# Performance work log

Measured on AMD Instinct MI355X. Metric: run time of the kernel, lower is better.

The kernel has to match this reference:

```python
import jax, jax.numpy as jnp
import numpy as np

EPS = 1e-8        # LinearGELU eps
LN_EPS = 1e-5     # LayerNorm eps
NUM_HEADS = 16
DIM = 1024
HIDDEN = 4096
B, N = 4, 785


def _lin(x, xj, w, lw, b=None, lb=None):
    # LinearLinear: primal linear + JVP wrt input and tangent params (lw, lb)
    y = x @ w.T
    yj = xj @ w.T + x @ lw.T
    if b is not None:
        y = y + b
    if lb is not None:
        yj = yj + lb
    return y, yj


def _ln(x, xj, w, b, lw, lb):
    # LinearLayerNorm forward + manual JVP (matches torch source exactly)
    mean = x.mean(-1, keepdims=True)
    xc = x - mean
    var = (xc * xc).mean(-1, keepdims=True)
    std = jnp.sqrt(var + LN_EPS)
    xhat = xc / std
    out = xhat * w + b
    t1 = xhat * lw + lb                              # tangent wrt affine params
    mj = xj.mean(-1, keepdims=True)
    xjc = xj - mj
    a = xjc * std
    corr = 2.0 * (xc * xjc).mean(-1, keepdims=True)
    bterm = (0.5 / std) * corr * xc
    c = (1.0 / std) ** 2 * (a - bterm)
    return out, t1 + c * w


def _gelu(x, xj):
    # exact (erf) GELU; jvp uses gelu(x)/(x+EPS) + x*pdf(x) as in source
    out = 0.5 * x * (1.0 + jax.lax.erf(x * np.float32(1.0 / np.sqrt(2.0))))
    pdf = jnp.exp(-0.5 * x * x) * np.float32(1.0 / np.sqrt(2.0 * np.pi))
    return out, xj * (out / (x + EPS) + x * pdf)


def _attn(x, xj, qkv_w, qkv_lw, proj_w, proj_b, proj_lw, proj_lb):
    Bb, Nn, C = x.shape
    H = NUM_HEADS
    D = C // H
    scale = np.float32(D) ** -0.5
    qkv, qkv_j = _lin(x, xj, qkv_w, qkv_lw)  # [B,N,3C], qkv_bias=False
    def split(t):
        return t.reshape(Bb, Nn, 3, H, D).transpose(2, 0, 3, 1, 4)
    q, k, v = split(qkv)
    qj, kj, vj = split(qkv_j)
    q = q * scale
    qj = qj * scale
    attn = jax.nn.softmax(jnp.einsum('bhnd,bhmd->bhnm', q, k), axis=-1)
    out = jnp.einsum('bhnm,bhmd->bhnd', attn, v)
    # softmax JVP: dm = A_jvp + B_jvp; filter = dm*attn - rowsum(dm*attn)*attn
    dm = jnp.einsum('bhnd,bhmd->bhnm', qj, k) + jnp.einsum('bhnd,bhmd->bhnm', q, kj)
    f = dm * attn
    filt = f - f.sum(-1, keepdims=True) * attn  # == diag(dm @ attn^T) * attn correction
    out_j = jnp.einsum('bhnm,bhmd->bhnd', filt, v) + jnp.einsum('bhnm,bhmd->bhnd', attn, vj)
    out = out.transpose(0, 2, 1, 3).reshape(Bb, Nn, C)
    out_j = out_j.transpose(0, 2, 1, 3).reshape(Bb, Nn, C)
    return _lin(out, out_j, proj_w, proj_lw, proj_b, proj_lb)


def setup_inputs() -> dict:
    keys = jax.random.split(jax.random.key(0), 32)
    ki = iter(keys)
    def nrm(shape, s=0.02):
        return (jax.random.normal(next(ki), shape, jnp.float32) * s).astype(jnp.float32)
    d, h = DIM, HIDDEN
    inp = {
        'input': jax.random.normal(next(ki), (B, N, d), jnp.float32),
        'input_jvp': jax.random.normal(next(ki), (B, N, d), jnp.float32),
        'n1_w': 1.0 + nrm((d,), 0.1), 'n1_b': nrm((d,), 0.1),
        'n1_lw': nrm((d,), 0.1), 'n1_lb': nrm((d,), 0.1),
        'qkv_w': nrm((3 * d, d)), 'qkv_lw': nrm((3 * d, d)),
        'proj_w': nrm((d, d)), 'proj_b': nrm((d,), 0.1),
        'proj_lw': nrm((d, d)), 'proj_lb': nrm((d,), 0.1),
        'n2_w': 1.0 + nrm((d,), 0.1), 'n2_b': nrm((d,), 0.1),
        'n2_lw': nrm((d,), 0.1), 'n2_lb': nrm((d,), 0.1),
        'fc1_w': nrm((h, d)), 'fc1_b': nrm((h,), 0.1),
        'fc1_lw': nrm((h, d)), 'fc1_lb': nrm((h,), 0.1),
        'fc2_w': nrm((d, h)), 'fc2_b': nrm((d,), 0.1),
        'fc2_lw': nrm((d, h)), 'fc2_lb': nrm((d,), 0.1),
    }
    return inp


def reference(input, input_jvp, n1_w, n1_b, n1_lw, n1_lb, qkv_w, qkv_lw,
              proj_w, proj_b, proj_lw, proj_lb, n2_w, n2_b, n2_lw, n2_lb,
              fc1_w, fc1_b, fc1_lw, fc1_lb, fc2_w, fc2_b, fc2_lw, fc2_lb):
    x, xj = _ln(input, input_jvp, n1_w, n1_b, n1_lw, n1_lb)
    x, xj = _attn(x, xj, qkv_w, qkv_lw, proj_w, proj_b, proj_lw, proj_lb)
    x = x + input
    xj = xj + input_jvp
    i2, i2j = x, xj
    x, xj = _ln(x, xj, n2_w, n2_b, n2_lw, n2_lb)
    x, xj = _lin(x, xj, fc1_w, fc1_lw, fc1_b, fc1_lb)
    x, xj = _gelu(x, xj)
    x, xj = _lin(x, xj, fc2_w, fc2_lw, fc2_b, fc2_lb)
    return (x + i2, xj + i2j)
```

## Files before the change

kernel.cpp:

```cpp
#include <hip/hip_runtime.h>
#include <hip/hip_bf16.h>

typedef unsigned short u16;
typedef unsigned int   u32;

#define MP     3328
#define MREAL  3140
#define DIMC   1024
#define H3C    3072
#define HIDC   4096
#define NKV    785
#define SLEN   896

typedef __bf16 bf16x8 __attribute__((ext_vector_type(8)));
typedef float  f32x4  __attribute__((ext_vector_type(4)));

#define MFMA(d,a,b) (d) = __builtin_amdgcn_mfma_f32_16x16x32_bf16((a),(b),(d),0,0,0)

__device__ __forceinline__ u16 f2bf(float f){
  u32 u = __builtin_bit_cast(u32, f);
  return (u16)((u + 0x7fffu + ((u >> 16) & 1u)) >> 16);
}
__device__ __forceinline__ float bf2f(u16 h){
  return __builtin_bit_cast(float, (u32)h << 16);
}
__device__ __forceinline__ void gload16(const u16* g, u16* l){
  __builtin_amdgcn_global_load_lds(
      (const __attribute__((address_space(1))) void*)g,
      (__attribute__((address_space(3))) void*)l, 16, 0, 0);
}
__device__ __forceinline__ float wsum(float v){
  #pragma unroll
  for (int o = 32; o >= 1; o >>= 1) v += __shfl_xor(v, o);
  return v;
}

__global__ __launch_bounds__(256) void cvt2_k(
    const float* __restrict__ in0, u16* __restrict__ out0, int n0,
    const float* __restrict__ in1, u16* __restrict__ out1, int n1)
{
  int i = (blockIdx.x * 256 + threadIdx.x) * 4;
  const float* src; u16* dst;
  if (i < n0){ src = in0 + i; dst = out0 + i; }
  else { int j = i - n0; if (j >= n1) return; src = in1 + j; dst = out1 + j; }
  float4 v = *(const float4*)src;
  ushort4 o4;
  o4.x = f2bf(v.x); o4.y = f2bf(v.y); o4.z = f2bf(v.z); o4.w = f2bf(v.w);
  *(ushort4*)dst = o4;
}

__global__ __launch_bounds__(256) void ln_jvp_k(
    const float* __restrict__ x, const float* __restrict__ xj,
    const float* __restrict__ w, const float* __restrict__ b,
    const float* __restrict__ lw, const float* __restrict__ lb,
    u16* __restrict__ out, u16* __restrict__ outj)
{
  const int row = blockIdx.x, t = threadIdx.x;
  const size_t ro = (size_t)row * DIMC;
  if (row >= MREAL){
    for (int i = t; i < DIMC; i += 256){ out[ro+i] = 0; outj[ro+i] = 0; }
    return;
  }
  const float4 v  = ((const float4*)(x  + ro))[t];
  const float4 vj = ((const float4*)(xj + ro))[t];
  float sx  = v.x+v.y+v.z+v.w;
  float sxx = v.x*v.x+v.y*v.y+v.z*v.z+v.w*v.w;
  float sj  = vj.x+vj.y+vj.z+vj.w;
  float sxj = v.x*vj.x+v.y*vj.y+v.z*vj.z+v.w*vj.w;
  __shared__ __attribute__((aligned(64))) float red[4][4];
  sx = wsum(sx); sxx = wsum(sxx); sj = wsum(sj); sxj = wsum(sxj);
  const int wid = t>>6, lane = t&63;
  if (lane == 0){ red[wid][0]=sx; red[wid][1]=sxx; red[wid][2]=sj; red[wid][3]=sxj; }
  __syncthreads();
  sx  = red[0][0]+red[1][0]+red[2][0]+red[3][0];
  sxx = red[0][1]+red[1][1]+red[2][1]+red[3][1];
  sj  = red[0][2]+red[1][2]+red[2][2]+red[3][2];
  sxj = red[0][3]+red[1][3]+red[2][3]+red[3][3];
  const float inv  = 1.0f/1024.0f;
  const float mean = sx*inv, meanj = sj*inv;
  const float var  = sxx*inv - mean*mean;
  const float cov  = sxj*inv - mean*meanj;
  const float rstd = rsqrtf(var + 1e-5f);
  const float r3   = rstd*rstd*rstd;
  const float4 wv  = ((const float4*)w)[t];
  const float4 bv  = ((const float4*)b)[t];
  const float4 lwv = ((const float4*)lw)[t];
  const float4 lbv = ((const float4*)lb)[t];
  const float xs[4]  = {v.x,v.y,v.z,v.w},   xjs[4] = {vj.x,vj.y,vj.z,vj.w};
  const float wss[4] = {wv.x,wv.y,wv.z,wv.w}, bs[4] = {bv.x,bv.y,bv.z,bv.w};
  const float lws[4] = {lwv.x,lwv.y,lwv.z,lwv.w}, lbs[4] = {lbv.x,lbv.y,lbv.z,lbv.w};
  const int i0 = t*4;
  #pragma unroll
  for (int e = 0; e < 4; e++){
    const float xc = xs[e]-mean, xjc = xjs[e]-meanj;
    const float xhat = xc*rstd;
    const float cc = xjc*rstd - xc*cov*r3;
    out [ro+i0+e] = f2bf(xhat*wss[e] + bs[e]);
    outj[ro+i0+e] = f2bf(xhat*lws[e] + lbs[e] + cc*wss[e]);
  }
}

template<int EPI>
__global__ __launch_bounds__(512, 1) void gemm_jvp_wide_k(
    const u16* __restrict__ A, const u16* __restrict__ Aj, int lda,
    const u16* __restrict__ B, const u16* __restrict__ Bj, int K,
    const float* __restrict__ bias, const float* __restrict__ biasj,
    void* __restrict__ Yv, void* __restrict__ Yjv, int ldy)
{
  __shared__ __attribute__((aligned(128))) u16 lds[3][24576];
  const int tid = threadIdx.x, wid = tid>>6, lane = tid&63;
  const int l4 = lane>>4, l15 = lane&15;
  const int ord = blockIdx.y * gridDim.x + blockIdx.x;
  const int cpx = (gridDim.x * gridDim.y) >> 3;
  const int nbk = (ord & 7) * cpx + (ord >> 3);
  const int m0 = (nbk / gridDim.x) * 256;
  const int n0 = (nbk % gridDim.x) * 128;
  f32x4 accY[4][4], accJ[4][4];
  #pragma unroll
  for (int i = 0; i < 4; i++)
    #pragma unroll
    for (int j = 0; j < 4; j++){
      accY[i][j] = (f32x4){0.f,0.f,0.f,0.f};
      accJ[i][j] = (f32x4){0.f,0.f,0.f,0.f};
    }
  const int boA0 = tid*16,        boA1 = (512+tid)*16;
  const int sbA0 = boA0 ^ (((boA0>>7)&7)<<4);
  const int sbA1 = boA1 ^ (((boA1>>7)&7)<<4);
  const int rA0 = sbA0>>6, cA0 = (sbA0&63)>>1;
  const int rA1 = sbA1>>6, cA1 = (sbA1&63)>>1;
  const int boB = tid*16;
  const int sbB = boB ^ (((boB>>7)&7)<<4);
  const int rB = sbB>>6, cB = (sbB&63)>>1;
  const u16* srcA0  = A  + (size_t)(m0+rA0)*lda + cA0;
  const u16* srcA1  = A  + (size_t)(m0+rA1)*lda + cA1;
  const u16* srcAj0 = Aj + (size_t)(m0+rA0)*lda + cA0;
  const u16* srcAj1 = Aj + (size_t)(m0+rA1)*lda + cA1;
  const u16* srcB   = B  + (size_t)(n0+rB)*K + cB;
  const u16* srcBj  = Bj + (size_t)(n0+rB)*K + cB;
  const int dA0 = tid*8, dA1 = (512+tid)*8, dB = tid*8;
  const int wr = wid>>1, wc = wid&1;
  int aoff[4], boff[4];
  #pragma unroll
  for (int i = 0; i < 4; i++){
    int ab_ = (wr*64 + i*16 + l15)*64 + l4*16;
    aoff[i] = ab_ ^ (((ab_>>7)&7)<<4);
    int bb_ = (wc*64 + i*16 + l15)*64 + l4*16;
    boff[i] = bb_ ^ (((bb_>>7)&7)<<4);
  }
  auto STAGE = [&](int buf, int t){
    const int k0 = t<<5;
    u16* Lb = &lds[buf][0];
    gload16(srcA0 +k0, Lb + dA0);
    gload16(srcA1 +k0, Lb + dA1);
    gload16(srcAj0+k0, Lb + 8192 + dA0);
    gload16(srcAj1+k0, Lb + 8192 + dA1);
    gload16(srcB  +k0, Lb + 16384 + dB);
    gload16(srcBj +k0, Lb + 20480 + dB);
  };
  const int nt = K >> 5;
  STAGE(0, 0);
  STAGE(1, 1);
  for (int t = 0; t < nt; t++){
    if (t + 1 < nt) asm volatile("s_waitcnt vmcnt(6)" ::: "memory");
    else            asm volatile("s_waitcnt vmcnt(0)" ::: "memory");
    __builtin_amdgcn_s_barrier();
    if (t + 2 < nt) STAGE((t+2)%3, t+2);
    const char* Lb = (const char*)&lds[t%3][0];
    bf16x8 af[4], ajf[4], bbf[4], bjf[4];
    #pragma unroll
    for (int i = 0; i < 4; i++){
      af[i]  = *(const bf16x8*)(Lb + aoff[i]);
      ajf[i] = *(const bf16x8*)(Lb + 16384 + aoff[i]);
      bbf[i] = *(const bf16x8*)(Lb + 32768 + boff[i]);
      bjf[i] = *(const bf16x8*)(Lb + 40960 + boff[i]);
    }
    __builtin_amdgcn_s_setprio(1);
    #pragma unroll
    for (int i = 0; i < 4; i++)
      #pragma unroll
      for (int j = 0; j < 4; j++){
        MFMA(accY[i][j], af[i],  bbf[j]);
        MFMA(accJ[i][j], ajf[i], bbf[j]);
        MFMA(accJ[i][j], af[i],  bjf[j]);
      }
    __builtin_amdgcn_s_setprio(0);
  }
  const int mb = m0 + wr*64 + (l4<<2);
  const int nb = n0 + wc*64 + l15;
  #pragma unroll
  for (int i = 0; i < 4; i++)
    #pragma unroll
    for (int j = 0; j < 4; j++)
      #pragma unroll
      for (int r = 0; r < 4; r++){
        const int m = mb + i*16 + r, n = nb + j*16;
        float y = accY[i][j][r], yj = accJ[i][j][r];
        if (EPI == 0){
          ((u16*)Yv )[(size_t)m*ldy+n] = f2bf(y);
          ((u16*)Yjv)[(size_t)m*ldy+n] = f2bf(yj);
        } else {
          y  += bias[n];
          yj += biasj[n];
          const float ge  = 0.5f*y*(1.0f + erff(y*0.70710678118654752f));
          const float pdf = __expf(-0.5f*y*y)*0.3989422804014327f;
          const float gj  = yj*(ge/(y + 1e-8f) + y*pdf);
          ((u16*)Yv )[(size_t)m*ldy+n] = f2bf(ge);
          ((u16*)Yjv)[(size_t)m*ldy+n] = f2bf(gj);
        }
      }
}

template<int EPI>
__global__ __launch_bounds__(256) void gemm_jvp_k(
    const u16* __restrict__ A, const u16* __restrict__ Aj, int lda,
    const u16* __restrict__ B, const u16* __restrict__ Bj, int K,
    const float* __restrict__ bias, const float* __restrict__ biasj,
    const float* __restrict__ res, const float* __restrict__ resj,
    void* __restrict__ Yv, void* __restrict__ Yjv, int ldy, int mwrite)
{
  __shared__ __attribute__((aligned(128))) u16 lds[3][4][128*32];
  const int tid = threadIdx.x, wid = tid>>6, lane = tid&63;
  const int ord = blockIdx.y * gridDim.x + blockIdx.x;
  const int cpx = (gridDim.x * gridDim.y) >> 3;
  const int nbk = (ord & 7) * cpx + (ord >> 3);
  const int m0 = (nbk / gridDim.x) * 128;
  const int n0 = (nbk % gridDim.x) * 128;
  f32x4 accY[4][4], accJ[4][4];
  #pragma unroll
  for (int i = 0; i < 4; i++)
    #pragma unroll
    for (int j = 0; j < 4; j++){
      accY[i][j] = (f32x4){0.f,0.f,0.f,0.f};
      accJ[i][j] = (f32x4){0.f,0.f,0.f,0.f};
    }
  const int bo0 = wid*1024 + lane*16;
  const int bo1 = bo0 + 4096;
  const int sb0 = bo0 ^ (((bo0>>7)&7)<<4);
  const int sb1 = bo1 ^ (((bo1>>7)&7)<<4);
  const int r0 = sb0>>6, c0 = (sb0&63)>>1;
  const int r1 = sb1>>6, c1 = (sb1&63)>>1;
  const u16* A0  = A  + (size_t)(m0+r0)*lda + c0;
  const u16* A1  = A  + (size_t)(m0+r1)*lda + c1;
  const u16* Aj0 = Aj + (size_t)(m0+r0)*lda + c0;
  const u16* Aj1 = Aj + (size_t)(m0+r1)*lda + c1;
  const u16* B0  = B  + (size_t)(n0+r0)*K + c0;
  const u16* B1  = B  + (size_t)(n0+r1)*K + c1;
  const u16* Bj0 = Bj + (size_t)(n0+r0)*K + c0;
  const u16* Bj1 = Bj + (size_t)(n0+r1)*K + c1;
  const int kq = (lane>>4)<<3;
  const int ar = (wid>>1)*64 + (lane&15);
  const int bc = (wid&1)*64 + (lane&15);
  int aoff[4], boff[4];
  #pragma unroll
  for (int i = 0; i < 4; i++){
    int ab_ = (ar+i*16)*64 + (kq<<1);
    aoff[i] = ab_ ^ (((ab_>>7)&7)<<4);
    int bb_ = (bc+i*16)*64 + (kq<<1);
    boff[i] = bb_ ^ (((bb_>>7)&7)<<4);
  }
  auto STAGE = [&](int buf, int t){
    const int k0 = t<<5;
    u16* p0 = &lds[buf][0][0];
    gload16(A0 +k0, p0+(bo0>>1)); gload16(A1 +k0, p0+(bo1>>1));
    u16* p1 = &lds[buf][1][0];
    gload16(Aj0+k0, p1+(bo0>>1)); gload16(Aj1+k0, p1+(bo1>>1));
    u16* p2 = &lds[buf][2][0];
    gload16(B0 +k0, p2+(bo0>>1)); gload16(B1 +k0, p2+(bo1>>1));
    u16* p3 = &lds[buf][3][0];
    gload16(Bj0+k0, p3+(bo0>>1)); gload16(Bj1+k0, p3+(bo1>>1));
  };
  const int nt = K >> 5;
  STAGE(0, 0);
  STAGE(1, 1);
  for (int t = 0; t < nt; t++){
    if (t + 1 < nt) asm volatile("s_waitcnt vmcnt(8)" ::: "memory");
    else            asm volatile("s_waitcnt vmcnt(0)" ::: "memory");
    __builtin_amdgcn_s_barrier();
    if (t + 2 < nt) STAGE((t+2)%3, t+2);
    const char* lAb  = (const char*)&lds[t%3][0][0];
    const char* lAjb = (const char*)&lds[t%3][1][0];
    const char* lBb  = (const char*)&lds[t%3][2][0];
    const char* lBjb = (const char*)&lds[t%3][3][0];
    bf16x8 af[4], ajf[4], bbf[4], bjf[4];
    #pragma unroll
    for (int i = 0; i < 4; i++){
      af[i]  = *(const bf16x8*)(lAb  + aoff[i]);
      ajf[i] = *(const bf16x8*)(lAjb + aoff[i]);
      bbf[i] = *(const bf16x8*)(lBb  + boff[i]);
      bjf[i] = *(const bf16x8*)(lBjb + boff[i]);
    }
    __builtin_amdgcn_s_setprio(1);
    #pragma unroll
    for (int i = 0; i < 4; i++)
      #pragma unroll
      for (int j = 0; j < 4; j++){
        MFMA(accY[i][j], af[i],  bbf[j]);
        MFMA(accJ[i][j], ajf[i], bbf[j]);
        MFMA(accJ[i][j], af[i],  bjf[j]);
      }
    __builtin_amdgcn_s_setprio(0);
  }
  const int mb = m0 + (wid>>1)*64 + ((lane>>4)<<2);
  const int nb = n0 + (wid&1)*64 + (lane&15);
  #pragma unroll
  for (int i = 0; i < 4; i++)
    #pragma unroll
    for (int j = 0; j < 4; j++)
      #pragma unroll
      for (int r = 0; r < 4; r++){
        const int m = mb + i*16 + r, n = nb + j*16;
        float y = accY[i][j][r], yj = accJ[i][j][r];
        if (EPI == 0){
          ((u16*)Yv )[(size_t)m*ldy+n] = f2bf(y);
          ((u16*)Yjv)[(size_t)m*ldy+n] = f2bf(yj);
        } else if (EPI == 1){
          if (m < mwrite){
            y  += bias[n]  + res [(size_t)m*ldy+n];
            yj += biasj[n] + resj[(size_t)m*ldy+n];
            ((float*)Yv )[(size_t)m*ldy+n] = y;
            ((float*)Yjv)[(size_t)m*ldy+n] = yj;
          }
        } else {
          y  += bias[n];
          yj += biasj[n];
          const float ge  = 0.5f*y*(1.0f + erff(y*0.70710678118654752f));
          const float pdf = __expf(-0.5f*y*y)*0.3989422804014327f;
          const float gj  = yj*(ge/(y + 1e-8f) + y*pdf);
          ((u16*)Yv )[(size_t)m*ldy+n] = f2bf(ge);
          ((u16*)Yjv)[(size_t)m*ldy+n] = f2bf(gj);
        }
      }
}

__global__ __launch_bounds__(256) void transpose_v_k(
    const u16* __restrict__ qkvb, const u16* __restrict__ qkvjb,
    u16* __restrict__ vT, u16* __restrict__ vjT)
{
  __shared__ __attribute__((aligned(64))) u16 tl[64][80];
  __shared__ __attribute__((aligned(64))) u16 tlj[64][80];
  const int kt = blockIdx.x, bh = blockIdx.y;
  const int b = bh>>4, h = bh&15;
  const int t = threadIdx.x;
  const int kv = t>>2, dd = (t&3)*16;
  const int kvg = kt*64 + kv;
  if (kvg < NKV){
    const u16* s0 = qkvb  + (size_t)(b*NKV+kvg)*H3C + 2048 + h*64 + dd;
    const u16* s1 = qkvjb + (size_t)(b*NKV+kvg)*H3C + 2048 + h*64 + dd;
    *(uint4*)&tl [kv][dd]   = *(const uint4*)s0;
    *(uint4*)&tl [kv][dd+8] = *(const uint4*)(s0+8);
    *(uint4*)&tlj[kv][dd]   = *(const uint4*)s1;
    *(uint4*)&tlj[kv][dd+8] = *(const uint4*)(s1+8);
  } else {
    uint4 z = {0,0,0,0};
    *(uint4*)&tl [kv][dd] = z; *(uint4*)&tl [kv][dd+8] = z;
    *(uint4*)&tlj[kv][dd] = z; *(uint4*)&tlj[kv][dd+8] = z;
  }
  __syncthreads();
  const int d = t>>2, kc = (t&3)*16;
  u16* d0 = vT  + ((size_t)bh*64 + d)*SLEN + kt*64 + kc;
  u16* d1 = vjT + ((size_t)bh*64 + d)*SLEN + kt*64 + kc;
  #pragma unroll
  for (int e = 0; e < 16; e++){ d0[e] = tl[kc+e][d]; d1[e] = tlj[kc+e][d]; }
}

__global__ __launch_bounds__(256) void flash_attn_jvp_k(
    const u16* __restrict__ qkvb, const u16* __restrict__ qkvjb,
    const u16* __restrict__ vT, const u16* __restrict__ vjT,
    u16* __restrict__ o, u16* __restrict__ oj)
{
  __shared__ __attribute__((aligned(128))) u16 lK  [2][64*64];
  __shared__ __attribute__((aligned(128))) u16 lKj [2][64*64];
  __shared__ __attribute__((aligned(128))) u16 lvT [64*64];
  __shared__ __attribute__((aligned(128))) u16 lvjT[64*64];
  __shared__ __attribute__((aligned(128))) u16 pl  [128*64];
  __shared__ __attribute__((aligned(128))) u16 pdl [128*64];
  const int tid = threadIdx.x, wid = tid>>6, lane = tid&63;
  const int l4 = lane>>4, l15 = lane&15;
  const int qt = blockIdx.x, bh = blockIdx.y, b = bh>>4, h = bh&15;

  bf16x8 qf[2][2], qjf[2][2];
  {
    const size_t qrb = (size_t)b*NKV + qt*128 + wid*32;
    #pragma unroll
    for (int i = 0; i < 2; i++){
      const size_t ro = (qrb + i*16 + l15)*H3C + h*64;
      #pragma unroll
      for (int ks = 0; ks < 2; ks++){
        qf [i][ks] = *(const bf16x8*)(qkvb  + ro + ks*32 + l4*8);
        qjf[i][ks] = *(const bf16x8*)(qkvjb + ro + ks*32 + l4*8);
      }
    }
  }
  float m_st[2][4], l_pt[2][4], g_pt[2][4];
  f32x4 PO[2][4], PTJ[2][4];
  #pragma unroll
  for (int i = 0; i < 2; i++)
    #pragma unroll
    for (int r = 0; r < 4; r++){
      m_st[i][r] = -1e30f; l_pt[i][r] = 0.f; g_pt[i][r] = 0.f;
    }
  #pragma unroll
  for (int i = 0; i < 2; i++)
    #pragma unroll
    for (int j = 0; j < 4; j++){
      PO[i][j] = (f32x4){0.f,0.f,0.f,0.f};
      PTJ[i][j] = (f32x4){0.f,0.f,0.f,0.f};
    }
  char* plb  = (char*)pl;
  char* pdlb = (char*)pdl;
  const char* lvTb  = (const char*)lvT;
  const char* lvjTb = (const char*)lvjT;

  const int g0 = tid, g1 = 256 + tid;
  const int row0 = g0>>3, cs0 = (g0&7) ^ (row0&7);
  const int row1 = g1>>3, cs1 = (g1&7) ^ (row1&7);
  auto stageK = [&](int buf, int t){
    const size_t k0 = (size_t)(b*NKV + t*64 + row0)*H3C + 1024 + h*64 + cs0*8;
    const size_t k1 = (size_t)(b*NKV + t*64 + row1)*H3C + 1024 + h*64 + cs1*8;
    gload16(qkvb  + k0, &lK [buf][0] + g0*8);
    gload16(qkvjb + k0, &lKj[buf][0] + g0*8);
    gload16(qkvb  + k1, &lK [buf][0] + g1*8);
    gload16(qkvjb + k1, &lKj[buf][0] + g1*8);
  };
  auto stageV = [&](int t){
    const size_t v0 = ((size_t)bh*64 + row0)*SLEN + t*64 + cs0*8;
    const size_t v1 = ((size_t)bh*64 + row1)*SLEN + t*64 + cs1*8;
    gload16(vT  + v0, lvT  + g0*8);
    gload16(vjT + v0, lvjT + g0*8);
    gload16(vT  + v1, lvT  + g1*8);
    gload16(vjT + v1, lvjT + g1*8);
  };

  stageK(0, 0);
  stageV(0);
  for (int t = 0; t < 13; t++){
    asm volatile("s_waitcnt vmcnt(4)" ::: "memory");
    __builtin_amdgcn_s_barrier();
    const char* lKb  = (const char*)&lK [t&1][0];
    const char* lKjb = (const char*)&lKj[t&1][0];

    #pragma unroll
    for (int i = 0; i < 2; i++){
      f32x4 s[4], dm[4];
      #pragma unroll
      for (int j = 0; j < 4; j++){
        s[j] = (f32x4){0.f,0.f,0.f,0.f};
        dm[j] = (f32x4){0.f,0.f,0.f,0.f};
      }
      #pragma unroll
      for (int ks = 0; ks < 2; ks++){
        #pragma unroll
        for (int j = 0; j < 4; j++){
          const int row = j*16 + l15;
          const int byt = (row*128 + ks*64 + l4*16) ^ ((row&7)<<4);
          const bf16x8 kf  = *(const bf16x8*)(lKb  + byt);
          const bf16x8 kjf = *(const bf16x8*)(lKjb + byt);
          MFMA(s[j],  qf[i][ks],  kf);
          MFMA(dm[j], qjf[i][ks], kf);
          MFMA(dm[j], qf[i][ks],  kjf);
        }
      }
      float tm[4] = {-1e30f,-1e30f,-1e30f,-1e30f};
      #pragma unroll
      for (int j = 0; j < 4; j++){
        const int colg = t*64 + j*16 + l15;
        #pragma unroll
        for (int r = 0; r < 4; r++){
          float sv = s[j][r]*0.125f;
          if (colg >= NKV) sv = -1e30f;
          s[j][r] = sv;
          dm[j][r] *= 0.125f;
          tm[r] = fmaxf(tm[r], sv);
        }
      }
      float vmax[4];
      bool need = false;
      #pragma unroll
      for (int r = 0; r < 4; r++){
        float v = tm[r];
        v = fmaxf(v, __shfl_xor(v, 1));
        v = fmaxf(v, __shfl_xor(v, 2));
        v = fmaxf(v, __shfl_xor(v, 4));
        v = fmaxf(v, __shfl_xor(v, 8));
        vmax[r] = v;
        need = need || (v > m_st[i][r] + 4.0f);
      }
      if (__any(need)){
        #pragma unroll
        for (int r = 0; r < 4; r++){
          const float nm = fmaxf(m_st[i][r], vmax[r]);
          const float sc = __expf(m_st[i][r] - nm);
          m_st[i][r] = nm;
          l_pt[i][r] *= sc;
          g_pt[i][r] *= sc;
          #pragma unroll
          for (int j = 0; j < 4; j++){ PO[i][j][r] *= sc; PTJ[i][j][r] *= sc; }
        }
      }
      #pragma unroll
      for (int j = 0; j < 4; j++){
        const int col = j*16 + l15;
        #pragma unroll
        for (int r = 0; r < 4; r++){
          const float p  = __expf(s[j][r] - m_st[i][r]);
          const float pd = p * dm[j][r];
          l_pt[i][r] += p;
          g_pt[i][r] += pd;
          const int row = wid*32 + i*16 + l4*4 + r;
          const int byt = (row*128 + col*2) ^ ((row&7)<<4);
          *(u16*)(plb  + byt) = f2bf(p);
          *(u16*)(pdlb + byt) = f2bf(pd);
        }
      }
    }

    if (t + 1 < 13) stageK((t+1)&1, t+1);
    if (t + 1 < 13) asm volatile("s_waitcnt vmcnt(4)" ::: "memory");
    else            asm volatile("s_waitcnt vmcnt(0)" ::: "memory");
    __builtin_amdgcn_s_barrier();

    #pragma unroll
    for (int ks = 0; ks < 2; ks++){
      bf16x8 pa[2], pda[2];
      #pragma unroll
      for (int i = 0; i < 2; i++){
        const int row = wid*32 + i*16 + l15;
        const int byt = (row*128 + ks*64 + l4*16) ^ ((row&7)<<4);
        pa[i]  = *(const bf16x8*)(plb  + byt);
        pda[i] = *(const bf16x8*)(pdlb + byt);
      }
      #pragma unroll
      for (int j = 0; j < 4; j++){
        const int row = j*16 + l15;
        const int byt = (row*128 + ks*64 + l4*16) ^ ((row&7)<<4);
        const bf16x8 vb  = *(const bf16x8*)(lvTb  + byt);
        const bf16x8 vjb = *(const bf16x8*)(lvjTb + byt);
        #pragma unroll
        for (int i = 0; i < 2; i++){
          MFMA(PO[i][j],  pa[i],  vb);
          MFMA(PTJ[i][j], pda[i], vb);
          MFMA(PTJ[i][j], pa[i],  vjb);
        }
      }
    }
    __builtin_amdgcn_s_barrier();
    if (t + 1 < 13) stageV(t+1);
  }

  #pragma unroll
  for (int i = 0; i < 2; i++)
    #pragma unroll
    for (int r = 0; r < 4; r++){
      float lv = l_pt[i][r], gv = g_pt[i][r];
      lv += __shfl_xor(lv, 1); gv += __shfl_xor(gv, 1);
      lv += __shfl_xor(lv, 2); gv += __shfl_xor(gv, 2);
      lv += __shfl_xor(lv, 4); gv += __shfl_xor(gv, 4);
      lv += __shfl_xor(lv, 8); gv += __shfl_xor(gv, 8);
      const int ql = qt*128 + wid*32 + i*16 + l4*4 + r;
      if (ql < NKV){
        const float rl = 1.0f / lv;
        const float gg = gv * rl;
        #pragma unroll
        for (int j = 0; j < 4; j++){
          const size_t oo = ((size_t)b*NKV + ql)*DIMC + h*64 + j*16 + l15;
          const float po = PO[i][j][r] * rl;
          o [oo] = f2bf(po);
          oj[oo] = f2bf(PTJ[i][j][r]*rl - gg*po);
        }
      }
    }
}

extern "C" void kernel_launch(void* const* d_in, const int* in_sizes, int n_in,
                              void* d_out, int out_size, void* d_ws, size_t ws_size,
                              hipStream_t stream)
{
  (void)in_sizes; (void)n_in; (void)out_size;
  const float* input   = (const float*)d_in[0];
  const float* inputj  = (const float*)d_in[1];
  const float* n1_w    = (const float*)d_in[2];
  const float* n1_b    = (const float*)d_in[3];
  const float* n1_lw   = (const float*)d_in[4];
  const float* n1_lb   = (const float*)d_in[5];
  const float* qkv_w   = (const float*)d_in[6];
  const float* qkv_lw  = (const float*)d_in[7];
  const float* proj_w  = (const float*)d_in[8];
  const float* proj_b  = (const float*)d_in[9];
  const float* proj_lw = (const float*)d_in[10];
  const float* proj_lb = (const float*)d_in[11];
  const float* n2_w    = (const float*)d_in[12];
  const float* n2_b    = (const float*)d_in[13];
  const float* n2_lw   = (const float*)d_in[14];
  const float* n2_lb   = (const float*)d_in[15];
  const float* fc1_w   = (const float*)d_in[16];
  const float* fc1_b   = (const float*)d_in[17];
  const float* fc1_lw  = (const float*)d_in[18];
  const float* fc1_lb  = (const float*)d_in[19];
  const float* fc2_w   = (const float*)d_in[20];
  const float* fc2_b   = (const float*)d_in[21];
  const float* fc2_lw  = (const float*)d_in[22];
  const float* fc2_lb  = (const float*)d_in[23];

  const size_t SZ_W      = 2u*4194304u*2u;
  const size_t SZ_ARENA1 = 2u*(size_t)MP*HIDC*2u;
  const size_t SZ_VT     = (size_t)64*64*SLEN*2u;
  const size_t SZ_ARENA2 = 2u*SZ_VT;
  const size_t SZ_ARENA3 = 2u*(size_t)MP*DIMC*2u;
  const size_t SZ_X2     = (size_t)MP*DIMC*4u;
  const size_t NEEDED = SZ_W + SZ_ARENA1 + SZ_ARENA2 + SZ_ARENA3 + 2u*SZ_X2 + 4096u;
  if (ws_size < NEEDED) return;

  char* base = (char*)d_ws;
  size_t off = 0;
  auto ab = [&](size_t bytes)->char*{
    char* p = base + off;
    off += bytes; off = (off + 255) & ~(size_t)255;
    return p;
  };
  char* Wslot  = ab(SZ_W);
  char* arena1 = ab(SZ_ARENA1);
  char* arena2 = ab(SZ_ARENA2);
  char* arena3 = ab(SZ_ARENA3);
  float* x2  = (float*)ab(SZ_X2);
  float* x2j = (float*)ab(SZ_X2);

  u16* wbuf  = (u16*)Wslot;
  u16* wjbuf = wbuf + 4194304;
  u16* qkvb  = (u16*)arena1;
  u16* qkvjb = qkvb + (size_t)MP*H3C;
  u16* hb    = (u16*)arena1;
  u16* hjb   = hb + (size_t)MP*HIDC;
  u16* vT    = (u16*)arena2;
  u16* vjT   = vT + (size_t)64*64*SLEN;
  u16* x3b   = (u16*)arena2;
  u16* x3jb  = x3b + (size_t)MP*DIMC;
  u16* x1b   = (u16*)arena3;
  u16* x1jb  = x1b + (size_t)MP*DIMC;
  u16* ob    = (u16*)arena3;
  u16* ojb   = ob + (size_t)MP*DIMC;

  auto cvt2 = [&](const float* s0, u16* d0, int n0,
                  const float* s1, u16* d1, int n1){
    cvt2_k<<<dim3((n0 + n1 + 1023)/1024), 256, 0, stream>>>(s0, d0, n0, s1, d1, n1);
  };

  ln_jvp_k<<<dim3(MP), 256, 0, stream>>>(input, inputj, n1_w, n1_b, n1_lw, n1_lb,
                                         x1b, x1jb);
  cvt2(qkv_w, wbuf, H3C*DIMC, qkv_lw, wjbuf, H3C*DIMC);
  gemm_jvp_wide_k<0><<<dim3(H3C/128, MP/256), 512, 0, stream>>>(
      x1b, x1jb, DIMC, wbuf, wjbuf, DIMC, nullptr, nullptr,
      qkvb, qkvjb, H3C);
  transpose_v_k<<<dim3(14, 64), 256, 0, stream>>>(qkvb, qkvjb, vT, vjT);
  flash_attn_jvp_k<<<dim3(7, 64), 256, 0, stream>>>(qkvb, qkvjb, vT, vjT, ob, ojb);
  cvt2(proj_w, wbuf, DIMC*DIMC, proj_lw, wjbuf, DIMC*DIMC);
  gemm_jvp_k<1><<<dim3(DIMC/128, MP/128), 256, 0, stream>>>(
      ob, ojb, DIMC, wbuf, wjbuf, DIMC, proj_b, proj_lb, input, inputj,
      x2, x2j, DIMC, MREAL);
  ln_jvp_k<<<dim3(MP), 256, 0, stream>>>(x2, x2j, n2_w, n2_b, n2_lw, n2_lb,
                                         x3b, x3jb);
  cvt2(fc1_w, wbuf, HIDC*DIMC, fc1_lw, wjbuf, HIDC*DIMC);
  gemm_jvp_wide_k<2><<<dim3(HIDC/128, MP/256), 512, 0, stream>>>(
      x3b, x3jb, DIMC, wbuf, wjbuf, DIMC, fc1_b, fc1_lb,
      hb, hjb, HIDC);
  cvt2(fc2_w, wbuf, DIMC*HIDC, fc2_lw, wjbuf, DIMC*HIDC);
  float* out0 = (float*)d_out;
  float* out1 = out0 + (size_t)MREAL*DIMC;
  gemm_jvp_k<1><<<dim3(DIMC/128, MP/128), 256, 0, stream>>>(
      hb, hjb, HIDC, wbuf, wjbuf, HIDC, fc2_b, fc2_lb, x2, x2j,
      out0, out1, DIMC, MREAL);
}
```

Measured before the change: 525.6 us.

## Load A-operand fragments directly from global into registers, staging only B in LDS

The JVP GEMM now stages only the B and Bj weight tiles through LDS. The A and Aj activation fragments are loaded straight from global memory into registers with inline global_load_dwordx4, using double-buffered register sets in a loop unrolled by two. This halves LDS footprint and LDS traffic per k-step and aims to raise occupancy. In exchange, A fragments are no longer shared across waves, so global/L2 traffic for A doubles, register pressure rises, and correctness relies on hand-tuned vmcnt counts and an even tile count.

Result: slower. 589.1 us (+12.1%).

```diff
diff --git a/kernel.cpp b/kernel.cpp
--- a/kernel.cpp
+++ b/kernel.cpp
@@ -28,6 +28,9 @@
   __builtin_amdgcn_global_load_lds(
       (const __attribute__((address_space(1))) void*)g,
       (__attribute__((address_space(3))) void*)l, 16, 0, 0);
+}
+__device__ __forceinline__ void gload_frag(bf16x8& d, const u16* p){
+  asm volatile("global_load_dwordx4 %0, %1, off" : "=v"(d) : "v"(p));
 }
 __device__ __forceinline__ float wsum(float v){
   #pragma unroll
@@ -218,8 +221,9 @@
     const float* __restrict__ res, const float* __restrict__ resj,
     void* __restrict__ Yv, void* __restrict__ Yjv, int ldy, int mwrite)
 {
-  __shared__ __attribute__((aligned(128))) u16 lds[3][4][128*32];
+  __shared__ __attribute__((aligned(128))) u16 lds[3][2][128*32];
   const int tid = threadIdx.x, wid = tid>>6, lane = tid&63;
+  const int l4 = lane>>4, l15 = lane&15;
   const int ord = blockIdx.y * gridDim.x + blockIdx.x;
   const int cpx = (gridDim.x * gridDim.y) >> 3;
   const int nbk = (ord & 7) * cpx + (ord >> 3);
@@ -233,59 +237,60 @@
       accY[i][j] = (f32x4){0.f,0.f,0.f,0.f};
       accJ[i][j] = (f32x4){0.f,0.f,0.f,0.f};
     }
-  const int bo0 = wid*1024 + lane*16;
-  const int bo1 = bo0 + 4096;
+  const int bo0 = tid*16, bo1 = 4096 + tid*16;
   const int sb0 = bo0 ^ (((bo0>>7)&7)<<4);
   const int sb1 = bo1 ^ (((bo1>>7)&7)<<4);
   const int r0 = sb0>>6, c0 = (sb0&63)>>1;
   const int r1 = sb1>>6, c1 = (sb1&63)>>1;
-  const u16* A0  = A  + (size_t)(m0+r0)*lda + c0;
-  const u16* A1  = A  + (size_t)(m0+r1)*lda + c1;
-  const u16* Aj0 = Aj + (size_t)(m0+r0)*lda + c0;
-  const u16* Aj1 = Aj + (size_t)(m0+r1)*lda + c1;
   const u16* B0  = B  + (size_t)(n0+r0)*K + c0;
   const u16* B1  = B  + (size_t)(n0+r1)*K + c1;
   const u16* Bj0 = Bj + (size_t)(n0+r0)*K + c0;
   const u16* Bj1 = Bj + (size_t)(n0+r1)*K + c1;
-  const int kq = (lane>>4)<<3;
-  const int ar = (wid>>1)*64 + (lane&15);
-  const int bc = (wid&1)*64 + (lane&15);
-  int aoff[4], boff[4];
+  const int ar = (wid>>1)*64 + l15;
+  const int kq = l4*8;
+  const u16* aptr [4];
+  const u16* ajptr[4];
   #pragma unroll
   for (int i = 0; i < 4; i++){
-    int ab_ = (ar+i*16)*64 + (kq<<1);
-    aoff[i] = ab_ ^ (((ab_>>7)&7)<<4);
+    aptr [i] = A  + (size_t)(m0+ar+i*16)*lda + kq;
+    ajptr[i] = Aj + (size_t)(m0+ar+i*16)*lda + kq;
+  }
+  const int bc = (wid&1)*64 + l15;
+  int boff[4];
+  #pragma unroll
+  for (int i = 0; i < 4; i++){
     int bb_ = (bc+i*16)*64 + (kq<<1);
     boff[i] = bb_ ^ (((bb_>>7)&7)<<4);
   }
-  auto STAGE = [&](int buf, int t){
+  auto STAGEB = [&](int buf, int t){
     const int k0 = t<<5;
-    u16* p0 = &lds[buf][0][0];
-    gload16(A0 +k0, p0+(bo0>>1)); gload16(A1 +k0, p0+(bo1>>1));
-    u16* p1 = &lds[buf][1][0];
-    gload16(Aj0+k0, p1+(bo0>>1)); gload16(Aj1+k0, p1+(bo1>>1));
-    u16* p2 = &lds[buf][2][0];
+    u16* p2 = &lds[buf][0][0];
     gload16(B0 +k0, p2+(bo0>>1)); gload16(B1 +k0, p2+(bo1>>1));
-    u16* p3 = &lds[buf][3][0];
+    u16* p3 = &lds[buf][1][0];
     gload16(Bj0+k0, p3+(bo0>>1)); gload16(Bj1+k0, p3+(bo1>>1));
   };
+  bf16x8 aFe[4], ajFe[4], aFo[4], ajFo[4];
+  auto LOADA = [&](int t, bf16x8 (&cA)[4], bf16x8 (&cAj)[4]){
+    const int k0 = t<<5;
+    #pragma unroll
+    for (int i = 0; i < 4; i++) gload_frag(cA[i],  aptr [i] + k0);
+    #pragma unroll
+    for (int i = 0; i < 4; i++) gload_frag(cAj[i], ajptr[i] + k0);
+  };
   const int nt = K >> 5;
-  STAGE(0, 0);
-  STAGE(1, 1);
-  for (int t = 0; t < nt; t++){
-    if (t + 1 < nt) asm volatile("s_waitcnt vmcnt(8)" ::: "memory");
-    else            asm volatile("s_waitcnt vmcnt(0)" ::: "memory");
+  STAGEB(0, 0); LOADA(0, aFe, ajFe);
+  STAGEB(1, 1); LOADA(1, aFo, ajFo);
+  auto BODY = [&](int t, bf16x8 (&cA)[4], bf16x8 (&cAj)[4]){
+    if (t + 1 < nt) asm volatile("s_waitcnt vmcnt(12)" ::: "memory");
+    else            asm volatile("s_waitcnt vmcnt(0)"  ::: "memory");
+    __builtin_amdgcn_sched_barrier(0);
     __builtin_amdgcn_s_barrier();
-    if (t + 2 < nt) STAGE((t+2)%3, t+2);
-    const char* lAb  = (const char*)&lds[t%3][0][0];
-    const char* lAjb = (const char*)&lds[t%3][1][0];
-    const char* lBb  = (const char*)&lds[t%3][2][0];
-    const char* lBjb = (const char*)&lds[t%3][3][0];
-    bf16x8 af[4], ajf[4], bbf[4], bjf[4];
+    if (t + 2 < nt) STAGEB((t+2)%3, t+2);
+    const char* lBb  = (const char*)&lds[t%3][0][0];
+    const char* lBjb = (const char*)&lds[t%3][1][0];
+    bf16x8 bbf[4], bjf[4];
     #pragma unroll
     for (int i = 0; i < 4; i++){
-      af[i]  = *(const bf16x8*)(lAb  + aoff[i]);
-      ajf[i] = *(const bf16x8*)(lAjb + aoff[i]);
       bbf[i] = *(const bf16x8*)(lBb  + boff[i]);
       bjf[i] = *(const bf16x8*)(lBjb + boff[i]);
     }
@@ -294,11 +299,16 @@
     for (int i = 0; i < 4; i++)
       #pragma unroll
       for (int j = 0; j < 4; j++){
-        MFMA(accY[i][j], af[i],  bbf[j]);
-        MFMA(accJ[i][j], ajf[i], bbf[j]);
-        MFMA(accJ[i][j], af[i],  bjf[j]);
+        MFMA(accY[i][j], cA[i],  bbf[j]);
+        MFMA(accJ[i][j], cAj[i], bbf[j]);
+        MFMA(accJ[i][j], cA[i],  bjf[j]);
       }
     __builtin_amdgcn_s_setprio(0);
+    if (t + 2 < nt) LOADA(t+2, cA, cAj);
+  };
+  for (int t = 0; t < nt; t += 2){
+    BODY(t,   aFe, ajFe);
+    BODY(t+1, aFo, ajFo);
   }
   const int mb = m0 + (wid>>1)*64 + ((lane>>4)<<2);
   const int nb = n0 + (wid&1)*64 + (lane&15);
```
